# Kernel tuning notes

Hardware: AMD Instinct MI355X
Metric: run time of the kernel (lower is better)

The kernel has to match this reference:

```python
import jax, jax.numpy as jnp
import numpy as np
from jax import lax

B = 16           # graphs per batch
N_PER = 4096     # points per graph (equal-sized graphs)
C_IN = 32        # in_channels
RATIO = 0.25
MAX_NBR = 32     # max_num_neighbors in radius()


def _xavier(key, fan_in, fan_out):
    lim = np.sqrt(6.0 / (fan_in + fan_out)).astype(np.float32)
    return jax.random.uniform(key, (fan_in, fan_out), jnp.float32, -lim, lim)


def setup_inputs() -> dict:
    key = jax.random.key(0)
    ks = jax.random.split(key, 16)
    x = jax.random.normal(ks[0], (B * N_PER, C_IN), jnp.float32)
    pos = jax.random.uniform(ks[1], (B * N_PER, 3), jnp.float32) * 20.0
    batch = jnp.repeat(jnp.arange(B, dtype=jnp.int64), N_PER)
    p = {
        'x': x, 'pos': pos, 'batch': batch,
        'scaler_mean': jnp.zeros((1, C_IN), jnp.float32),
        'scaler_std': jnp.ones((1, C_IN), jnp.float32),
        # SA1: Linear(32+3,64) -> Sigmoid -> Linear(64,128)
        'sa1_w1': _xavier(ks[2], C_IN + 3, 64), 'sa1_b1': jnp.zeros((64,), jnp.float32),
        'sa1_w2': _xavier(ks[3], 64, 128),      'sa1_b2': jnp.zeros((128,), jnp.float32),
        # SA2: Linear(128+3,128) -> Sigmoid -> Linear(128,256)
        'sa2_w1': _xavier(ks[4], 128 + 3, 128), 'sa2_b1': jnp.zeros((128,), jnp.float32),
        'sa2_w2': _xavier(ks[5], 128, 256),     'sa2_b2': jnp.zeros((256,), jnp.float32),
        # Global SA: Linear(256+3,256) -> Sigmoid -> Linear(256,512)
        'g_w1': _xavier(ks[6], 256 + 3, 256),   'g_b1': jnp.zeros((256,), jnp.float32),
        'g_w2': _xavier(ks[7], 256, 512),       'g_b2': jnp.zeros((512,), jnp.float32),
        # fc: Linear(512,256) -> Sigmoid -> Linear(256,128)
        'fc_w1': _xavier(ks[8], 512, 256),      'fc_b1': jnp.zeros((256,), jnp.float32),
        'fc_w2': _xavier(ks[9], 256, 128),      'fc_b2': jnp.zeros((128,), jnp.float32),
    }
    return p


def _fps(pos, k):
    # Farthest point sampling, deterministic start at index 0. pos: [B, n, 3] -> idx [B, k]
    pos = lax.stop_gradient(pos)
    d0 = jnp.sum((pos - pos[:, :1, :]) ** 2, -1)  # [B, n] dist^2 to start point

    def step(mind, _):
        nxt = jnp.argmax(mind, axis=1)                                  # [B]
        p = jnp.take_along_axis(pos, nxt[:, None, None], axis=1)        # [B,1,3]
        mind = jnp.minimum(mind, jnp.sum((pos - p) ** 2, -1))
        return mind, nxt

    _, rest = lax.scan(step, d0, None, length=k - 1)                    # [k-1, B]
    start = jnp.zeros((1, pos.shape[0]), rest.dtype)
    return jnp.concatenate([start, rest], 0).T                          # [B, k]


def _gather_nbr(v, nbr):
    # v: [B, n, C], nbr: [B, k, MAX_NBR] -> [B, k, MAX_NBR, C]
    return jax.vmap(lambda vb, nb: vb[nb])(v, nbr)


def _sa_module(x, pos, w1, b1, w2, b2, ratio, r):
    # PointNetConv (max aggregation) over a radius graph from FPS centers.
    Bb, n, _ = x.shape
    k = int(n * ratio)
    idx = _fps(pos, k)                                                  # [B, k]
    pos_dst = jnp.take_along_axis(pos, idx[:, :, None], axis=1)         # [B, k, 3]
    d2 = jnp.sum((pos_dst[:, :, None, :] - pos[:, None, :, :]) ** 2, -1)  # [B,k,n]
    masked = jnp.where(d2 <= r * r, d2, jnp.inf)
    negv, nbr = lax.top_k(-masked, MAX_NBR)                             # nearest <=32 within radius
    valid = jnp.isfinite(negv)                                          # [B,k,32]
    x_j = _gather_nbr(x, nbr)                                           # [B,k,32,C]
    rel = _gather_nbr(pos, nbr) - pos_dst[:, :, None, :]                # pos_j - pos_i
    feat = jnp.concatenate([x_j, rel], axis=-1)
    msg = jax.nn.sigmoid(feat @ w1 + b1) @ w2 + b2                      # [B,k,32,2h]
    msg = jnp.where(valid[..., None], msg, -jnp.inf)
    agg = jnp.max(msg, axis=2)                                          # max aggregation
    agg = jnp.where(jnp.isfinite(agg), agg, 0.0)  # (self is always a neighbor, defensive)
    return jax.nn.relu(agg), pos_dst


def reference(x, pos, batch, scaler_mean, scaler_std,
              sa1_w1, sa1_b1, sa1_w2, sa1_b2,
              sa2_w1, sa2_b1, sa2_w2, sa2_b2,
              g_w1, g_b1, g_w2, g_b2,
              fc_w1, fc_b1, fc_w2, fc_b2):
    x = (x - scaler_mean) / scaler_std
    xb = x.reshape(B, N_PER, -1)      # batch is sorted with N_PER points per graph
    pb = pos.reshape(B, N_PER, 3)
    xb, pb = _sa_module(xb, pb, sa1_w1, sa1_b1, sa1_w2, sa1_b2, RATIO, 2.0)
    xb, pb = _sa_module(xb, pb, sa2_w1, sa2_b1, sa2_w2, sa2_b2, RATIO, 4.0)
    # GlobalSAModule: relu(nn(cat[x, pos])) then global max pool
    h = jnp.concatenate([xb, pb], axis=-1)
    h = jax.nn.relu(jax.nn.sigmoid(h @ g_w1 + g_b1) @ g_w2 + g_b2)      # [B, 256, 512]
    g = jnp.max(h, axis=1)                                              # [B, 512]
    out = jax.nn.sigmoid(g @ fc_w1 + fc_b1) @ fc_w2 + fc_b2
    return jax.nn.relu(out)                                             # last_act='relu'
```

## Files before the change

kernel.cpp:

```cpp
#include <hip/hip_runtime.h>
#include <hip/hip_bf16.h>
#include <math.h>

namespace {

constexpr int NB   = 16;
constexpr int N1   = 4096;
constexpr int K1   = 1024;
constexpr int K2   = 256;
constexpr int MAXN = 32;
constexpr int RCAP = 448;

__device__ __forceinline__ float sigmoidf_(float x) {
  return 1.0f / (1.0f + __expf(-x));
}

__device__ __forceinline__ float readlane_f(float v, int l) {
  return __int_as_float(__builtin_amdgcn_readlane(__float_as_int(v), l));
}


#define FPS_DPP_STEP(CTRL)                                                     \
  {                                                                            \
    const unsigned olo =                                                       \
        (unsigned)__builtin_amdgcn_update_dpp(0, (int)lo, (CTRL), 0xF, 0xF, true); \
    const unsigned ohi =                                                       \
        (unsigned)__builtin_amdgcn_update_dpp(0, (int)hi, (CTRL), 0xF, 0xF, true); \
    const unsigned long long o = ((unsigned long long)ohi << 32) | olo;        \
    const unsigned long long cur = ((unsigned long long)hi << 32) | lo;        \
    if (o > cur) { lo = olo; hi = ohi; }                                       \
  }

template<int NPT>
__device__ __forceinline__ void fps_run(
    const float* __restrict__ sx, const float* __restrict__ sy,
    const float* __restrict__ sz, int k,
    float* __restrict__ dgx, float* __restrict__ dgy, float* __restrict__ dgz,
    int* readyp, unsigned long long (*red)[4]) {
  const int t = threadIdx.x;
  const int lane = t & 63, wave = t >> 6;
  float px[NPT], py[NPT], pz[NPT], mind[NPT];
  unsigned niv[NPT];
  const float c0x = sx[0], c0y = sy[0], c0z = sz[0];
  unsigned long long best = 0;
#pragma unroll
  for (int i = 0; i < NPT; i++) {
    const int p = i * 256 + t;
    niv[i] = ~(unsigned)p;
    px[i] = sx[p]; py[i] = sy[p]; pz[i] = sz[p];
    const float dx = px[i] - c0x, dy = py[i] - c0y, dz = pz[i] - c0z;
    const float d2 = dx * dx + dy * dy + dz * dz;
    mind[i] = d2;
    const unsigned long long cand =
        ((unsigned long long)__float_as_uint(d2) << 32) | niv[i];
    if (cand > best) best = cand;
  }
  if (t == 0) { dgx[0] = c0x; dgy[0] = c0y; dgz[0] = c0z; }
  for (int it = 1; it < k; it++) {
    unsigned lo = (unsigned)best, hi = (unsigned)(best >> 32);
    FPS_DPP_STEP(0x111)
    FPS_DPP_STEP(0x112)
    FPS_DPP_STEP(0x114)
    FPS_DPP_STEP(0x118)
    FPS_DPP_STEP(0x142)
    FPS_DPP_STEP(0x143)
    const int par = it & 1;
    if (lane == 63) red[par][wave] = ((unsigned long long)hi << 32) | lo;
    __syncthreads();
    const unsigned long long w0 = red[par][0], w1 = red[par][1];
    const unsigned long long w2 = red[par][2], w3 = red[par][3];
    const unsigned long long m01 = w0 > w1 ? w0 : w1;
    const unsigned long long m23 = w2 > w3 ? w2 : w3;
    const unsigned long long win = m01 > m23 ? m01 : m23;
    const int p = (int)(~(unsigned)win);
    const float nx = sx[p], ny = sy[p], nz = sz[p];
    if (t == 0) {
      dgx[it] = nx; dgy[it] = ny; dgz[it] = nz;
      if ((it & 3) == 3)
        __hip_atomic_store(readyp, it + 1, __ATOMIC_RELEASE,
                           __HIP_MEMORY_SCOPE_AGENT);
    }
    best = 0;
#pragma unroll
    for (int i = 0; i < NPT; i++) {
      const float dx = px[i] - nx, dy = py[i] - ny, dz = pz[i] - nz;
      const float d2 = dx * dx + dy * dy + dz * dz;
      const float m = fminf(mind[i], d2);
      mind[i] = m;
      const unsigned long long cand =
          ((unsigned long long)__float_as_uint(m) << 32) | niv[i];
      if (cand > best) best = cand;
    }
  }
  if (t == 0)
    __hip_atomic_store(readyp, k, __ATOMIC_RELEASE, __HIP_MEMORY_SCOPE_AGENT);
}

#undef FPS_DPP_STEP

struct RadSmem {
  float candd[4][RCAP];
  int   candi[4][RCAP];
};

__device__ __forceinline__ void radius_lds(
    const float* __restrict__ px, const float* __restrict__ py,
    const float* __restrict__ pz, int N,
    float cx, float cy, float cz, float r2,
    RadSmem& sm, int* nb, int* cntp, int wave, int lane) {
  int total = 0;
  for (int base = 0; base < N; base += 64) {
    const int p = base + lane;
    const float dx = px[p] - cx;
    const float dy = py[p] - cy;
    const float dz = pz[p] - cz;
    const float d2 = dx * dx + dy * dy + dz * dz;
    const bool pred = d2 <= r2;
    const unsigned long long m = __ballot(pred);
    if (pred) {
      const int slot = total + __popcll(m & ((1ull << lane) - 1ull));
      if (slot < RCAP) { sm.candd[wave][slot] = d2; sm.candi[wave][slot] = p; }
    }
    total += __popcll(m);
  }
  if (total > RCAP) total = RCAP;
  if (total <= MAXN) {
    if (lane < total) nb[lane] = sm.candi[wave][lane];
  } else {
    for (int jj = 0; jj < MAXN; jj++) {
      float bvd = INFINITY; int bvi = 0x7fffffff; int bslot = 0;
      for (int s = lane; s < total; s += 64) {
        const float d = sm.candd[wave][s];
        const int i = sm.candi[wave][s];
        if (d < bvd || (d == bvd && i < bvi)) { bvd = d; bvi = i; bslot = s; }
      }
#pragma unroll
      for (int off = 32; off; off >>= 1) {
        const float od = __shfl_xor(bvd, off);
        const int   oi = __shfl_xor(bvi, off);
        const int   os = __shfl_xor(bslot, off);
        if (od < bvd || (od == bvd && oi < bvi)) { bvd = od; bvi = oi; bslot = os; }
      }
      if (lane == 0) { nb[jj] = bvi; sm.candd[wave][bslot] = INFINITY; }
    }
  }
  if (lane == 0) *cntp = (total < MAXN) ? total : MAXN;
}

template<int CIN_T, int H, int COUT, bool SCALE>
__device__ __forceinline__ void conv_center(
    const float* __restrict__ xin,
    const float* __restrict__ ptsx, const float* __restrict__ ptsy,
    const float* __restrict__ ptsz,
    float ctrx, float ctry, float ctrz,
    const int* nb, int V,
    const float* __restrict__ w1, const float* __restrict__ b1,
    const float* __restrict__ w2, const float* __restrict__ b2,
    const float* __restrict__ smean, const float* __restrict__ sstd,
    float* __restrict__ outrow, float* part ) {
  constexpr int FIN  = CIN_T + 3;
  constexpr int KREG = (FIN + 63) / 64;
  constexpr int HREG = H / 64;
  constexpr int CREG = COUT / 64;
  constexpr int RPW  = MAXN / 4;
  const int t = threadIdx.x, lane = t & 63, wave = t >> 6;
  float m[CREG];
#pragma unroll
  for (int ck = 0; ck < CREG; ck++) m[ck] = -INFINITY;
  if (V > wave * RPW) {
    float sm = 0.0f, sd = 1.0f;
    if (SCALE && lane < CIN_T) { sm = smean[lane]; sd = sstd[lane]; }
    float fr[RPW][KREG];
#pragma unroll
    for (int r = 0; r < RPW; r++) {
      const int j = wave * RPW + r;
      const int p = (j < V) ? nb[j] : nb[0];
#pragma unroll
      for (int k2 = 0; k2 < KREG; k2++) {
        const int f = k2 * 64 + lane;
        float v = 0.0f;
        if (f < CIN_T) {
          v = xin[(size_t)p * CIN_T + f];
          if constexpr (SCALE) v = (v - sm) / sd;
        } else if (f < FIN) {
          const int d = f - CIN_T;
          const float pv = (d == 0 ? ptsx : (d == 1 ? ptsy : ptsz))[p];
          v = pv - (d == 0 ? ctrx : (d == 1 ? ctry : ctrz));
        }
        fr[r][k2] = v;
      }
    }
    float hh[RPW][HREG];
    {
      float acc[RPW][HREG];
#pragma unroll
      for (int r = 0; r < RPW; r++)
#pragma unroll
        for (int q = 0; q < HREG; q++) acc[r][q] = 0.0f;
#pragma unroll
      for (int k2 = 0; k2 < KREG; k2++) {
        const int lim = (FIN - k2 * 64) < 64 ? (FIN - k2 * 64) : 64;
        for (int fl = 0; fl < lim; fl++) {
          const int f = k2 * 64 + fl;
          float wv[HREG];
          if constexpr (HREG == 1) {
            wv[0] = w1[(size_t)f * H + lane];
          } else {
            const float2 w = *reinterpret_cast<const float2*>(
                &w1[(size_t)f * H + lane * 2]);
            wv[0] = w.x; wv[1] = w.y;
          }
#pragma unroll
          for (int r = 0; r < RPW; r++) {
            const float s = readlane_f(fr[r][k2], fl);
#pragma unroll
            for (int q = 0; q < HREG; q++) acc[r][q] = fmaf(s, wv[q], acc[r][q]);
          }
        }
      }
#pragma unroll
      for (int q = 0; q < HREG; q++) {
        const float bb = b1[lane * HREG + q];
#pragma unroll
        for (int r = 0; r < RPW; r++) hh[r][q] = sigmoidf_(acc[r][q] + bb);
      }
    }
    float acc2[RPW][CREG];
#pragma unroll
    for (int r = 0; r < RPW; r++)
#pragma unroll
      for (int q = 0; q < CREG; q++) acc2[r][q] = 0.0f;
    for (int hl = 0; hl < 64; hl++) {
#pragma unroll
      for (int q1 = 0; q1 < HREG; q1++) {
        const int h = hl * HREG + q1;
        float wv[CREG];
        if constexpr (CREG == 2) {
          const float2 w = *reinterpret_cast<const float2*>(
              &w2[(size_t)h * COUT + lane * 2]);
          wv[0] = w.x; wv[1] = w.y;
        } else {
          const float4 w = *reinterpret_cast<const float4*>(
              &w2[(size_t)h * COUT + lane * 4]);
          wv[0] = w.x; wv[1] = w.y; wv[2] = w.z; wv[3] = w.w;
        }
#pragma unroll
        for (int r = 0; r < RPW; r++) {
          const float s = readlane_f(hh[r][q1], hl);
#pragma unroll
          for (int q = 0; q < CREG; q++) acc2[r][q] = fmaf(s, wv[q], acc2[r][q]);
        }
      }
    }
#pragma unroll
    for (int r = 0; r < RPW; r++) {
      if (wave * RPW + r < V) {
#pragma unroll
        for (int q = 0; q < CREG; q++) m[q] = fmaxf(m[q], acc2[r][q]);
      }
    }
  }
#pragma unroll
  for (int q = 0; q < CREG; q++) part[wave * COUT + lane * CREG + q] = m[q];
  __syncthreads();
  if (t < COUT) {
    const float mm = fmaxf(fmaxf(part[0 * COUT + t], part[1 * COUT + t]),
                           fmaxf(part[2 * COUT + t], part[3 * COUT + t]));
    const float o = mm + b2[t];
    outrow[t] = o > 0.0f ? o : 0.0f;
  }
}

__global__ __launch_bounds__(256) void phase1_kernel(
    const float* __restrict__ pos, const float* __restrict__ x,
    const float* __restrict__ smean, const float* __restrict__ sstd,
    const float* __restrict__ s1w1, const float* __restrict__ s1b1,
    const float* __restrict__ s1w2, const float* __restrict__ s1b2,
    float* __restrict__ pxg, float* __restrict__ pyg, float* __restrict__ pzg,
    float* __restrict__ d1x, float* __restrict__ d1y, float* __restrict__ d1z,
    float* __restrict__ x1, unsigned int* __restrict__ gout,
    int* __restrict__ ctrl) {
  __shared__ __align__(16) char smem[49152];
  __shared__ __align__(16) unsigned long long red[2][4];
  __shared__ int s_item;
  const int t = threadIdx.x, lane = t & 63, wave = t >> 6;
  if (blockIdx.x < (unsigned)NB) {
    const int b = blockIdx.x;
    gout[b * 512 + t] = 0u;
    gout[b * 512 + t + 256] = 0u;
    float* sx = (float*)smem; float* sy = sx + N1; float* sz = sy + N1;
    const float* pb = pos + (size_t)b * N1 * 3;
    for (int p = t; p < N1; p += 256) {
      sx[p] = pb[p * 3 + 0]; sy[p] = pb[p * 3 + 1]; sz[p] = pb[p * 3 + 2];
    }
    __syncthreads();
    for (int p = t; p < N1; p += 256) {
      pxg[(size_t)b * N1 + p] = sx[p];
      pyg[(size_t)b * N1 + p] = sy[p];
      pzg[(size_t)b * N1 + p] = sz[p];
    }
    fps_run<N1 / 256>(sx, sy, sz, K1,
                      d1x + (size_t)b * K1, d1y + (size_t)b * K1,
                      d1z + (size_t)b * K1, &ctrl[8 + b], red);
    __syncthreads();
  }
  RadSmem& rs = *reinterpret_cast<RadSmem*>(smem);
  int* nb_l = reinterpret_cast<int*>(smem + sizeof(RadSmem));
  int* cnt_l = nb_l + 4 * MAXN;
  float* part = reinterpret_cast<float*>(cnt_l + 4);
  constexpr int NITEMS = NB * (K1 / 4);
  for (;;) {
    if (t == 0) s_item = atomicAdd(&ctrl[0], 1);
    __syncthreads();
    const int item = s_item;
    __syncthreads();
    if (item >= NITEMS) break;
    const int b = item % NB, grp = item / NB;
    if (t == 0) {
      while (__hip_atomic_load(&ctrl[8 + b], __ATOMIC_ACQUIRE,
                               __HIP_MEMORY_SCOPE_AGENT) < 4 * grp + 4)
        __builtin_amdgcn_s_sleep(16);
    }
    __syncthreads();
    const size_t pB = (size_t)b * N1, cB = (size_t)b * K1;
    const int ci = 4 * grp + wave;
    radius_lds(pxg + pB, pyg + pB, pzg + pB, N1,
               d1x[cB + ci], d1y[cB + ci], d1z[cB + ci], 4.0f,
               rs, nb_l + wave * MAXN, &cnt_l[wave], wave, lane);
    __syncthreads();
    for (int cc = 0; cc < 4; cc++) {
      const int c2 = 4 * grp + cc;
      conv_center<32, 64, 128, true>(
          x + pB * 32, pxg + pB, pyg + pB, pzg + pB,
          d1x[cB + c2], d1y[cB + c2], d1z[cB + c2],
          nb_l + cc * MAXN, cnt_l[cc],
          s1w1, s1b1, s1w2, s1b2, smean, sstd,
          x1 + (cB + c2) * 128, part);
      __syncthreads();
    }
  }
}

__global__ __launch_bounds__(256) void rad2conv2_kernel(
    const float* __restrict__ x1,
    const float* __restrict__ d1x, const float* __restrict__ d1y,
    const float* __restrict__ d1z,
    const float* __restrict__ s2w1, const float* __restrict__ s2b1,
    const float* __restrict__ s2w2, const float* __restrict__ s2b2,
    float* __restrict__ x2) {
  __shared__ __align__(16) RadSmem rs;
  __shared__ int nb_l[4 * MAXN];
  __shared__ int cnt_l[4];
  __shared__ __align__(16) float part[4 * 256];
  const int t = threadIdx.x, lane = t & 63, wave = t >> 6;
  const int b = blockIdx.x % NB, grp = blockIdx.x / NB;
  const size_t cB = (size_t)b * K1;
  const int ci = 4 * grp + wave;
  radius_lds(d1x + cB, d1y + cB, d1z + cB, K1,
             d1x[cB + ci], d1y[cB + ci], d1z[cB + ci], 16.0f,
             rs, nb_l + wave * MAXN, &cnt_l[wave], wave, lane);
  __syncthreads();
  for (int cc = 0; cc < 4; cc++) {
    const int c2 = 4 * grp + cc;
    conv_center<128, 128, 256, false>(
        x1 + cB * 128, d1x + cB, d1y + cB, d1z + cB,
        d1x[cB + c2], d1y[cB + c2], d1z[cB + c2],
        nb_l + cc * MAXN, cnt_l[cc],
        s2w1, s2b1, s2w2, s2b2, nullptr, nullptr,
        x2 + ((size_t)b * K2 + c2) * 256, part);
    __syncthreads();
  }
}

__global__ __launch_bounds__(256) void global_sa_kernel(
    const float* __restrict__ x2,
    const float* __restrict__ d1x, const float* __restrict__ d1y,
    const float* __restrict__ d1z,
    const float* __restrict__ gw1, const float* __restrict__ gb1,
    const float* __restrict__ gw2, const float* __restrict__ gb2,
    unsigned int* __restrict__ gout) {
  __shared__ float fin[4][259];
  __shared__ float s[4][256];
  const int t = threadIdx.x;
  const int blk = blockIdx.x;
  const int b = blk / 64;
  const int p0 = (blk % 64) * 4;
  for (int item = t; item < 4 * 259; item += 256) {
    const int p = item / 259, f = item - p * 259;
    float v;
    if (f < 256) {
      v = x2[((size_t)b * 256 + p0 + p) * 256 + f];
    } else {
      const int d = f - 256;
      v = (d == 0 ? d1x : (d == 1 ? d1y : d1z))[(size_t)b * K1 + p0 + p];
    }
    fin[p][f] = v;
  }
  __syncthreads();
  float acc[4] = {0.f, 0.f, 0.f, 0.f};
  for (int f = 0; f < 259; f++) {
    const float w = gw1[f * 256 + t];
#pragma unroll
    for (int p = 0; p < 4; p++) acc[p] = fmaf(fin[p][f], w, acc[p]);
  }
  const float bb = gb1[t];
#pragma unroll
  for (int p = 0; p < 4; p++) s[p][t] = sigmoidf_(acc[p] + bb);
  __syncthreads();
  float a0[4] = {0.f, 0.f, 0.f, 0.f}, a1[4] = {0.f, 0.f, 0.f, 0.f};
  for (int h = 0; h < 256; h++) {
    const float w0 = gw2[h * 512 + t];
    const float w1v = gw2[h * 512 + t + 256];
#pragma unroll
    for (int p = 0; p < 4; p++) {
      a0[p] = fmaf(s[p][h], w0, a0[p]);
      a1[p] = fmaf(s[p][h], w1v, a1[p]);
    }
  }
  const float b0 = gb2[t], b1v = gb2[t + 256];
  float m0 = 0.0f, m1 = 0.0f;
#pragma unroll
  for (int p = 0; p < 4; p++) {
    m0 = fmaxf(m0, fmaxf(a0[p] + b0, 0.0f));
    m1 = fmaxf(m1, fmaxf(a1[p] + b1v, 0.0f));
  }
  atomicMax(&gout[b * 512 + t], __float_as_uint(m0));
  atomicMax(&gout[b * 512 + t + 256], __float_as_uint(m1));
}

__global__ __launch_bounds__(256) void fc_kernel(
    const unsigned int* __restrict__ g,
    const float* __restrict__ fw1, const float* __restrict__ fb1,
    const float* __restrict__ fw2, const float* __restrict__ fb2,
    float* __restrict__ out) {
  __shared__ float gv[512];
  __shared__ float s[256];
  const int b = blockIdx.x, t = threadIdx.x;
  gv[t] = __uint_as_float(g[b * 512 + t]);
  gv[t + 256] = __uint_as_float(g[b * 512 + t + 256]);
  __syncthreads();
  float acc = 0.0f;
  for (int h = 0; h < 512; h++) acc = fmaf(gv[h], fw1[h * 256 + t], acc);
  s[t] = sigmoidf_(acc + fb1[t]);
  __syncthreads();
  if (t < 128) {
    float a2 = 0.0f;
    for (int h = 0; h < 256; h++) a2 = fmaf(s[h], fw2[h * 128 + t], a2);
    const float o = a2 + fb2[t];
    out[b * 128 + t] = o > 0.0f ? o : 0.0f;
  }
}

}

extern "C" void kernel_launch(void* const* d_in, const int* in_sizes, int n_in,
                              void* d_out, int out_size, void* d_ws, size_t ws_size,
                              hipStream_t stream) {
  (void)in_sizes; (void)n_in; (void)out_size; (void)ws_size;
  const float* x     = (const float*)d_in[0];
  const float* pos   = (const float*)d_in[1];
  const float* smean = (const float*)d_in[3];
  const float* sstd  = (const float*)d_in[4];
  const float* s1w1  = (const float*)d_in[5];
  const float* s1b1  = (const float*)d_in[6];
  const float* s1w2  = (const float*)d_in[7];
  const float* s1b2  = (const float*)d_in[8];
  const float* s2w1  = (const float*)d_in[9];
  const float* s2b1  = (const float*)d_in[10];
  const float* s2w2  = (const float*)d_in[11];
  const float* s2b2  = (const float*)d_in[12];
  const float* gw1   = (const float*)d_in[13];
  const float* gb1   = (const float*)d_in[14];
  const float* gw2   = (const float*)d_in[15];
  const float* gb2   = (const float*)d_in[16];
  const float* fw1   = (const float*)d_in[17];
  const float* fb1   = (const float*)d_in[18];
  const float* fw2   = (const float*)d_in[19];
  const float* fb2   = (const float*)d_in[20];

  char* ws = (char*)d_ws;
  size_t off = 0;
  auto take = [&](size_t bytes) -> char* {
    char* p = ws + off;
    off = (off + bytes + 255) & ~(size_t)255;
    return p;
  };
  float* pxg         = (float*)take((size_t)NB * N1 * 4);
  float* pyg         = (float*)take((size_t)NB * N1 * 4);
  float* pzg         = (float*)take((size_t)NB * N1 * 4);
  float* d1x         = (float*)take((size_t)NB * K1 * 4);
  float* d1y         = (float*)take((size_t)NB * K1 * 4);
  float* d1z         = (float*)take((size_t)NB * K1 * 4);
  float* x1          = (float*)take((size_t)NB * K1 * 128 * 4);
  float* x2          = (float*)take((size_t)NB * K2 * 256 * 4);
  unsigned int* gbuf = (unsigned int*)take((size_t)NB * 512 * 4);
  int* ctrl          = (int*)take(128);

  hipMemsetAsync(ctrl, 0, 128, stream);

  {
    void* args[] = {
        (void*)&pos, (void*)&x, (void*)&smean, (void*)&sstd,
        (void*)&s1w1, (void*)&s1b1, (void*)&s1w2, (void*)&s1b2,
        (void*)&pxg, (void*)&pyg, (void*)&pzg,
        (void*)&d1x, (void*)&d1y, (void*)&d1z,
        (void*)&x1, (void*)&gbuf, (void*)&ctrl};
    hipLaunchCooperativeKernel((void*)phase1_kernel, dim3(256), dim3(256),
                               args, 0, stream);
  }
  hipLaunchKernelGGL(rad2conv2_kernel, dim3(NB * K2 / 4), dim3(256), 0, stream,
                     x1, d1x, d1y, d1z, s2w1, s2b1, s2w2, s2b2, x2);
  hipLaunchKernelGGL(global_sa_kernel, dim3(NB * 64), dim3(256), 0, stream,
                     x2, d1x, d1y, d1z, gw1, gb1, gw2, gb2, gbuf);
  hipLaunchKernelGGL(fc_kernel, dim3(NB), dim3(256), 0, stream,
                     gbuf, fw1, fb1, fw2, fb2, (float*)d_out);
}
```

Before: 1.252 ms.

## Split cooperative FPS+conv kernel into separate FPS and radius/conv launches

Replaces the persistent cooperative kernel, which overlapped the FPS producers with radius/conv consumers through atomic ready flags, with a standalone FPS kernel followed by a normal grid launch for radius+conv1. FPS now buffers selected points in LDS and writes them out at the end. It also splits the per-thread argmax into two independent accumulators to shorten the dependency chain. This drops the polling, the atomics and the cooperative launch, but gives up the overlap of conv1 with the serial FPS loop, so conv1 only starts once FPS has finished.

```diff
diff --git a/kernel.cpp b/kernel.cpp
--- a/kernel.cpp
+++ b/kernel.cpp
@@ -32,17 +32,18 @@
   }
 
 template<int NPT>
-__device__ __forceinline__ void fps_run(
+__device__ __forceinline__ void fps_level(
     const float* __restrict__ sx, const float* __restrict__ sy,
     const float* __restrict__ sz, int k,
-    float* __restrict__ dgx, float* __restrict__ dgy, float* __restrict__ dgz,
-    int* readyp, unsigned long long (*red)[4]) {
+    float* __restrict__ selx, float* __restrict__ sely,
+    float* __restrict__ selz,
+    unsigned long long (*red)[4]) {
   const int t = threadIdx.x;
   const int lane = t & 63, wave = t >> 6;
   float px[NPT], py[NPT], pz[NPT], mind[NPT];
   unsigned niv[NPT];
   const float c0x = sx[0], c0y = sy[0], c0z = sz[0];
-  unsigned long long best = 0;
+  unsigned long long bestA = 0, bestB = 0;
 #pragma unroll
   for (int i = 0; i < NPT; i++) {
     const int p = i * 256 + t;
@@ -53,10 +54,12 @@
     mind[i] = d2;
     const unsigned long long cand =
         ((unsigned long long)__float_as_uint(d2) << 32) | niv[i];
-    if (cand > best) best = cand;
-  }
-  if (t == 0) { dgx[0] = c0x; dgy[0] = c0y; dgz[0] = c0z; }
+    if (i & 1) { if (cand > bestB) bestB = cand; }
+    else       { if (cand > bestA) bestA = cand; }
+  }
+  if (t == 0) { selx[0] = c0x; sely[0] = c0y; selz[0] = c0z; }
   for (int it = 1; it < k; it++) {
+    const unsigned long long best = bestA > bestB ? bestA : bestB;
     unsigned lo = (unsigned)best, hi = (unsigned)(best >> 32);
     FPS_DPP_STEP(0x111)
     FPS_DPP_STEP(0x112)
@@ -74,13 +77,8 @@
     const unsigned long long win = m01 > m23 ? m01 : m23;
     const int p = (int)(~(unsigned)win);
     const float nx = sx[p], ny = sy[p], nz = sz[p];
-    if (t == 0) {
-      dgx[it] = nx; dgy[it] = ny; dgz[it] = nz;
-      if ((it & 3) == 3)
-        __hip_atomic_store(readyp, it + 1, __ATOMIC_RELEASE,
-                           __HIP_MEMORY_SCOPE_AGENT);
-    }
-    best = 0;
+    if (t == 0) { selx[it] = nx; sely[it] = ny; selz[it] = nz; }
+    bestA = 0; bestB = 0;
 #pragma unroll
     for (int i = 0; i < NPT; i++) {
       const float dx = px[i] - nx, dy = py[i] - ny, dz = pz[i] - nz;
@@ -89,14 +87,44 @@
       mind[i] = m;
       const unsigned long long cand =
           ((unsigned long long)__float_as_uint(m) << 32) | niv[i];
-      if (cand > best) best = cand;
-    }
-  }
-  if (t == 0)
-    __hip_atomic_store(readyp, k, __ATOMIC_RELEASE, __HIP_MEMORY_SCOPE_AGENT);
+      if (i & 1) { if (cand > bestB) bestB = cand; }
+      else       { if (cand > bestA) bestA = cand; }
+    }
+  }
 }
 
 #undef FPS_DPP_STEP
+
+__global__ __launch_bounds__(256) void fps_l1_kernel(
+    const float* __restrict__ pos,
+    float* __restrict__ pxg, float* __restrict__ pyg, float* __restrict__ pzg,
+    float* __restrict__ d1x, float* __restrict__ d1y, float* __restrict__ d1z,
+    unsigned int* __restrict__ gout) {
+  __shared__ float sx[N1], sy[N1], sz[N1];
+  __shared__ float s2x[K1], s2y[K1], s2z[K1];
+  __shared__ __align__(16) unsigned long long red[2][4];
+  const int b = blockIdx.x;
+  const int t = threadIdx.x;
+  gout[b * 512 + t] = 0u;
+  gout[b * 512 + t + 256] = 0u;
+  const float* pb = pos + (size_t)b * N1 * 3;
+  for (int p = t; p < N1; p += 256) {
+    sx[p] = pb[p * 3 + 0]; sy[p] = pb[p * 3 + 1]; sz[p] = pb[p * 3 + 2];
+  }
+  __syncthreads();
+  fps_level<N1 / 256>(sx, sy, sz, K1, s2x, s2y, s2z, red);
+  __syncthreads();
+  for (int p = t; p < N1; p += 256) {
+    pxg[(size_t)b * N1 + p] = sx[p];
+    pyg[(size_t)b * N1 + p] = sy[p];
+    pzg[(size_t)b * N1 + p] = sz[p];
+  }
+  for (int i = t; i < K1; i += 256) {
+    d1x[(size_t)b * K1 + i] = s2x[i];
+    d1y[(size_t)b * K1 + i] = s2y[i];
+    d1z[(size_t)b * K1 + i] = s2z[i];
+  }
+}
 
 struct RadSmem {
   float candd[4][RCAP];
@@ -271,73 +299,37 @@
   }
 }
 
-__global__ __launch_bounds__(256) void phase1_kernel(
-    const float* __restrict__ pos, const float* __restrict__ x,
-    const float* __restrict__ smean, const float* __restrict__ sstd,
+__global__ __launch_bounds__(256) void rad1conv1_kernel(
+    const float* __restrict__ x,
+    const float* __restrict__ pxg, const float* __restrict__ pyg,
+    const float* __restrict__ pzg,
+    const float* __restrict__ d1x, const float* __restrict__ d1y,
+    const float* __restrict__ d1z,
     const float* __restrict__ s1w1, const float* __restrict__ s1b1,
     const float* __restrict__ s1w2, const float* __restrict__ s1b2,
-    float* __restrict__ pxg, float* __restrict__ pyg, float* __restrict__ pzg,
-    float* __restrict__ d1x, float* __restrict__ d1y, float* __restrict__ d1z,
-    float* __restrict__ x1, unsigned int* __restrict__ gout,
-    int* __restrict__ ctrl) {
-  __shared__ __align__(16) char smem[49152];
-  __shared__ __align__(16) unsigned long long red[2][4];
-  __shared__ int s_item;
+    const float* __restrict__ smean, const float* __restrict__ sstd,
+    float* __restrict__ x1) {
+  __shared__ __align__(16) RadSmem rs;
+  __shared__ int nb_l[4 * MAXN];
+  __shared__ int cnt_l[4];
+  __shared__ __align__(16) float part[4 * 128];
   const int t = threadIdx.x, lane = t & 63, wave = t >> 6;
-  if (blockIdx.x < (unsigned)NB) {
-    const int b = blockIdx.x;
-    gout[b * 512 + t] = 0u;
-    gout[b * 512 + t + 256] = 0u;
-    float* sx = (float*)smem; float* sy = sx + N1; float* sz = sy + N1;
-    const float* pb = pos + (size_t)b * N1 * 3;
-    for (int p = t; p < N1; p += 256) {
-      sx[p] = pb[p * 3 + 0]; sy[p] = pb[p * 3 + 1]; sz[p] = pb[p * 3 + 2];
-    }
+  const int b = blockIdx.x / (K1 / 4), grp = blockIdx.x % (K1 / 4);
+  const size_t pB = (size_t)b * N1, cB = (size_t)b * K1;
+  const int ci = 4 * grp + wave;
+  radius_lds(pxg + pB, pyg + pB, pzg + pB, N1,
+             d1x[cB + ci], d1y[cB + ci], d1z[cB + ci], 4.0f,
+             rs, nb_l + wave * MAXN, &cnt_l[wave], wave, lane);
+  __syncthreads();
+  for (int cc = 0; cc < 4; cc++) {
+    const int c2 = 4 * grp + cc;
+    conv_center<32, 64, 128, true>(
+        x + pB * 32, pxg + pB, pyg + pB, pzg + pB,
+        d1x[cB + c2], d1y[cB + c2], d1z[cB + c2],
+        nb_l + cc * MAXN, cnt_l[cc],
+        s1w1, s1b1, s1w2, s1b2, smean, sstd,
+        x1 + (cB + c2) * 128, part);
     __syncthreads();
-    for (int p = t; p < N1; p += 256) {
-      pxg[(size_t)b * N1 + p] = sx[p];
-      pyg[(size_t)b * N1 + p] = sy[p];
-      pzg[(size_t)b * N1 + p] = sz[p];
-    }
-    fps_run<N1 / 256>(sx, sy, sz, K1,
-                      d1x + (size_t)b * K1, d1y + (size_t)b * K1,
-                      d1z + (size_t)b * K1, &ctrl[8 + b], red);
-    __syncthreads();
-  }
-  RadSmem& rs = *reinterpret_cast<RadSmem*>(smem);
-  int* nb_l = reinterpret_cast<int*>(smem + sizeof(RadSmem));
-  int* cnt_l = nb_l + 4 * MAXN;
-  float* part = reinterpret_cast<float*>(cnt_l + 4);
-  constexpr int NITEMS = NB * (K1 / 4);
-  for (;;) {
-    if (t == 0) s_item = atomicAdd(&ctrl[0], 1);
-    __syncthreads();
-    const int item = s_item;
-    __syncthreads();
-    if (item >= NITEMS) break;
-    const int b = item % NB, grp = item / NB;
-    if (t == 0) {
-      while (__hip_atomic_load(&ctrl[8 + b], __ATOMIC_ACQUIRE,
-                               __HIP_MEMORY_SCOPE_AGENT) < 4 * grp + 4)
-        __builtin_amdgcn_s_sleep(16);
-    }
-    __syncthreads();
-    const size_t pB = (size_t)b * N1, cB = (size_t)b * K1;
-    const int ci = 4 * grp + wave;
-    radius_lds(pxg + pB, pyg + pB, pzg + pB, N1,
-               d1x[cB + ci], d1y[cB + ci], d1z[cB + ci], 4.0f,
-               rs, nb_l + wave * MAXN, &cnt_l[wave], wave, lane);
-    __syncthreads();
-    for (int cc = 0; cc < 4; cc++) {
-      const int c2 = 4 * grp + cc;
-      conv_center<32, 64, 128, true>(
-          x + pB * 32, pxg + pB, pyg + pB, pzg + pB,
-          d1x[cB + c2], d1y[cB + c2], d1z[cB + c2],
-          nb_l + cc * MAXN, cnt_l[cc],
-          s1w1, s1b1, s1w2, s1b2, smean, sstd,
-          x1 + (cB + c2) * 128, part);
-      __syncthreads();
-    }
   }
 }
 
@@ -353,7 +345,7 @@
   __shared__ int cnt_l[4];
   __shared__ __align__(16) float part[4 * 256];
   const int t = threadIdx.x, lane = t & 63, wave = t >> 6;
-  const int b = blockIdx.x % NB, grp = blockIdx.x / NB;
+  const int b = blockIdx.x / (K2 / 4), grp = blockIdx.x % (K2 / 4);
   const size_t cB = (size_t)b * K1;
   const int ci = 4 * grp + wave;
   radius_lds(d1x + cB, d1y + cB, d1z + cB, K1,
@@ -494,20 +486,12 @@
   float* x1          = (float*)take((size_t)NB * K1 * 128 * 4);
   float* x2          = (float*)take((size_t)NB * K2 * 256 * 4);
   unsigned int* gbuf = (unsigned int*)take((size_t)NB * 512 * 4);
-  int* ctrl          = (int*)take(128);
-
-  hipMemsetAsync(ctrl, 0, 128, stream);
-
-  {
-    void* args[] = {
-        (void*)&pos, (void*)&x, (void*)&smean, (void*)&sstd,
-        (void*)&s1w1, (void*)&s1b1, (void*)&s1w2, (void*)&s1b2,
-        (void*)&pxg, (void*)&pyg, (void*)&pzg,
-        (void*)&d1x, (void*)&d1y, (void*)&d1z,
-        (void*)&x1, (void*)&gbuf, (void*)&ctrl};
-    hipLaunchCooperativeKernel((void*)phase1_kernel, dim3(256), dim3(256),
-                               args, 0, stream);
-  }
+
+  hipLaunchKernelGGL(fps_l1_kernel, dim3(NB), dim3(256), 0, stream,
+                     pos, pxg, pyg, pzg, d1x, d1y, d1z, gbuf);
+  hipLaunchKernelGGL(rad1conv1_kernel, dim3(NB * K1 / 4), dim3(256), 0, stream,
+                     x, pxg, pyg, pzg, d1x, d1y, d1z,
+                     s1w1, s1b1, s1w2, s1b2, smean, sstd, x1);
   hipLaunchKernelGGL(rad2conv2_kernel, dim3(NB * K2 / 4), dim3(256), 0, stream,
                      x1, d1x, d1y, d1z, s2w1, s2b1, s2w2, s2b2, x2);
   hipLaunchKernelGGL(global_sa_kernel, dim3(NB * 64), dim3(256), 0, stream,
```

Result: faster. 1.208 ms (-3.5%).
